# Optimization experiments

Measured on AMD Instinct MI355X. Metric: run time of the kernel, lower is better.

## Reference

```python
import jax, jax.numpy as jnp
import numpy as np

B, N, D, DH = 2, 256, 256, 256


def setup_inputs() -> dict:
    key = jax.random.key(0)
    ks = jax.random.split(key, 8)
    s = 1.0 / np.sqrt(D)
    return {
        "x": jax.random.normal(ks[0], (B, N, D), dtype=jnp.float32),
        "e": jax.random.normal(ks[1], (B, N, N, D), dtype=jnp.float32),
        "Wq": jax.random.normal(ks[2], (D, DH), dtype=jnp.float32) * s,
        "bq": jnp.zeros((DH,), dtype=jnp.float32),
        "Wk": jax.random.normal(ks[3], (D, DH), dtype=jnp.float32) * s,
        "bk": jnp.zeros((DH,), dtype=jnp.float32),
        "Wv": jax.random.normal(ks[4], (D, DH), dtype=jnp.float32) * s,
        "bv": jnp.zeros((DH,), dtype=jnp.float32),
    }


def reference(x, e, Wq, bq, Wk, bk, Wv, bv):
    # Q_edge: [B, N, N, DH]; indexed Q[b, j, i, :]
    Q = jnp.einsum("bjid,dh->bjih", e, Wq) + bq
    K = x @ Wk + bk  # [B, N, DH]
    V = x @ Wv + bv  # [B, N, DH]
    scale = 1.0 / jnp.sqrt(jnp.asarray(Q.shape[-1], Q.dtype))
    # K_i[b,j,i] = K[b,i];  K_j[b,j,i] = K[b,j]  (torch expand semantics)
    att_i = jnp.exp(jnp.einsum("bjih,bih->bji", Q, K) * scale)
    att_j = jnp.exp(jnp.einsum("bjih,bjh->bji", Q, K) * scale)
    att_sum = att_i + att_j
    ai = att_i / att_sum  # dropout with p=0.0 is identity
    aj = att_j / att_sum
    # e_out[b,j,i] = ai*V[b,i] + aj*V[b,j]
    e_out = ai[..., None] * V[:, None, :, :] + aj[..., None] * V[:, :, None, :]
    return (x, e_out)
```

## Files before the change

### kernel.cpp

```cpp
#include <hip/hip_runtime.h>
#include <hip/hip_bf16.h>

constexpr int Bc  = 2;
constexpr int Nc  = 256;
constexpr int Dc  = 256;
constexpr int DHc = 256;
constexpr int BM  = 64;
constexpr int NIB = Nc / BM;

__global__ __launch_bounds__(256)
void prep_gvc(const float* __restrict__ x,
              const float* __restrict__ Wq, const float* __restrict__ bq,
              const float* __restrict__ Wk, const float* __restrict__ bk,
              const float* __restrict__ Wv, const float* __restrict__ bv,
              float* __restrict__ G, float* __restrict__ V, float* __restrict__ cc) {
    constexpr int RPB = 4;
    constexpr float scale = 0.0625f;
    __shared__ float xs[RPB][Dc];
    __shared__ float ks[RPB][DHc];
    const int r0 = blockIdx.x * RPB;
    const int dd = threadIdx.x;

    #pragma unroll
    for (int rr = 0; rr < RPB; ++rr)
        xs[rr][dd] = x[(size_t)(r0 + rr) * Dc + dd];
    __syncthreads();

    float ka[RPB], va[RPB];
    {
        float bkv = bk[dd], bvv = bv[dd];
        #pragma unroll
        for (int rr = 0; rr < RPB; ++rr) { ka[rr] = bkv; va[rr] = bvv; }
    }
    #pragma unroll 4
    for (int d0 = 0; d0 < Dc; ++d0) {
        float wk = Wk[(size_t)d0 * DHc + dd];
        float wv = Wv[(size_t)d0 * DHc + dd];
        #pragma unroll
        for (int rr = 0; rr < RPB; ++rr) {
            ka[rr] += xs[rr][d0] * wk;
            va[rr] += xs[rr][d0] * wv;
        }
    }
    #pragma unroll
    for (int rr = 0; rr < RPB; ++rr) {
        ks[rr][dd] = ka[rr];
        V[(size_t)(r0 + rr) * DHc + dd] = va[rr];
    }
    __syncthreads();

    float ga[RPB] = {};
    #pragma unroll 8
    for (int h = 0; h < DHc; ++h) {
        float wq = Wq[(size_t)dd * DHc + h];
        #pragma unroll
        for (int rr = 0; rr < RPB; ++rr) ga[rr] += ks[rr][h] * wq;
    }
    #pragma unroll
    for (int rr = 0; rr < RPB; ++rr)
        G[(size_t)(r0 + rr) * Dc + dd] = ga[rr] * scale;

    {
        int rr = dd >> 6, l = dd & 63;
        float p = 0.f;
        #pragma unroll
        for (int k = 0; k < 4; ++k) p += ks[rr][l + 64 * k] * bq[l + 64 * k];
        #pragma unroll
        for (int m = 1; m < 64; m <<= 1) p += __shfl_xor(p, m, 64);
        if (l == 0) cc[r0 + rr] = p * scale;
    }
}

__global__ __launch_bounds__(256)
void edge_main(const float* __restrict__ e,
               const float* __restrict__ G,
               const float* __restrict__ V,
               const float* __restrict__ cc,
               float* __restrict__ eout) {
    const int bid = blockIdx.x;
    const int b   = bid / (Nc * NIB);
    const int rem = bid % (Nc * NIB);
    const int j   = rem / NIB;
    const int i0  = (rem % NIB) * BM;
    const int tid = threadIdx.x;
    const int l   = tid & 63;
    const int w   = tid >> 6;

    const size_t nbase = (size_t)b * Nc;
    const float4 gj = *reinterpret_cast<const float4*>(G + (nbase + j) * Dc + l * 4);
    const float4 vj = *reinterpret_cast<const float4*>(V + (nbase + j) * DHc + l * 4);
    const float  cj = cc[nbase + j];

    const int ibase = i0 + w * 16;
    const float4* erow = reinterpret_cast<const float4*>(
        e + (((size_t)b * Nc + j) * Nc + ibase) * Dc) + l;
    const float4* Grow = reinterpret_cast<const float4*>(G + (nbase + ibase) * Dc) + l;
    const float4* Vrow = reinterpret_cast<const float4*>(V + (nbase + ibase) * DHc) + l;
    float4* orow = reinterpret_cast<float4*>(
        eout + (((size_t)b * Nc + j) * Nc + ibase) * Dc) + l;
    const float* ccp = cc + nbase + ibase;

    #pragma unroll 4
    for (int t = 0; t < 16; ++t) {
        float4 ev = erow[(size_t)t * 64];
        float4 gi = Grow[(size_t)t * 64];
        float si = ev.x * gi.x + ev.y * gi.y + ev.z * gi.z + ev.w * gi.w;
        float sj = ev.x * gj.x + ev.y * gj.y + ev.z * gj.z + ev.w * gj.w;
        #pragma unroll
        for (int m = 1; m < 64; m <<= 1) {
            si += __shfl_xor(si, m, 64);
            sj += __shfl_xor(sj, m, 64);
        }
        si += ccp[t];
        sj += cj;
        float ai = 1.f / (1.f + __expf(sj - si));
        float aj = 1.f - ai;
        float4 vi = Vrow[(size_t)t * 64];
        float4 o;
        o.x = ai * vi.x + aj * vj.x;
        o.y = ai * vi.y + aj * vj.y;
        o.z = ai * vi.z + aj * vj.z;
        o.w = ai * vi.w + aj * vj.w;
        orow[(size_t)t * 64] = o;
    }
}

extern "C" void kernel_launch(void* const* d_in, const int* in_sizes, int n_in,
                              void* d_out, int out_size, void* d_ws, size_t ws_size,
                              hipStream_t stream) {
    const float* x  = (const float*)d_in[0];
    const float* e  = (const float*)d_in[1];
    const float* Wq = (const float*)d_in[2];
    const float* bq = (const float*)d_in[3];
    const float* Wk = (const float*)d_in[4];
    const float* bk = (const float*)d_in[5];
    const float* Wv = (const float*)d_in[6];
    const float* bv = (const float*)d_in[7];
    float* out = (float*)d_out;

    float* G  = (float*)d_ws;
    float* V  = G + (size_t)Bc * Nc * Dc;
    float* cc = V + (size_t)Bc * Nc * DHc;

    hipMemcpyAsync(out, x, (size_t)Bc * Nc * Dc * sizeof(float),
                   hipMemcpyDeviceToDevice, stream);

    prep_gvc<<<Bc * Nc / 4, 256, 0, stream>>>(x, Wq, bq, Wk, bk, Wv, bv, G, V, cc);
    edge_main<<<Bc * Nc * NIB, 256, 0, stream>>>(
        e, G, V, cc, out + (size_t)Bc * Nc * Dc);
}
```

Before: 306.6 us.

## Split wavefronts into quarter-row groups with register prefetch and nontemporal stores

Each wavefront now handles four rows at once, with 16 lanes per row holding four float4 chunks each. This shrinks the cross-lane reduction from 6 to 4 shuffle steps. The next rows' e and G values are prefetched into registers while the current row is computed. Outputs are written with nontemporal stores to avoid polluting the cache with streaming data. The device-to-device memcpy of x is replaced by a small copy kernel launched after the main kernel. Together these aim to cut launch/copy overhead and memory latency stalls, at the cost of higher register pressure.

Result: faster. 295.0 us (-3.8%).

```diff
diff --git a/kernel.cpp b/kernel.cpp
--- a/kernel.cpp
+++ b/kernel.cpp
@@ -1,5 +1,7 @@
 #include <hip/hip_runtime.h>
 #include <hip/hip_bf16.h>
+
+typedef float nt4 __attribute__((ext_vector_type(4)));
 
 constexpr int Bc  = 2;
 constexpr int Nc  = 256;
@@ -72,6 +74,12 @@
 }
 
 __global__ __launch_bounds__(256)
+void copy_x(const float4* __restrict__ in, float4* __restrict__ out) {
+    int i = blockIdx.x * 256 + threadIdx.x;
+    out[i] = in[i];
+}
+
+__global__ __launch_bounds__(256)
 void edge_main(const float* __restrict__ e,
                const float* __restrict__ G,
                const float* __restrict__ V,
@@ -85,43 +93,80 @@
     const int tid = threadIdx.x;
     const int l   = tid & 63;
     const int w   = tid >> 6;
+    const int g   = l >> 4;
+    const int c4  = l & 15;
 
     const size_t nbase = (size_t)b * Nc;
-    const float4 gj = *reinterpret_cast<const float4*>(G + (nbase + j) * Dc + l * 4);
-    const float4 vj = *reinterpret_cast<const float4*>(V + (nbase + j) * DHc + l * 4);
-    const float  cj = cc[nbase + j];
+    const float4* G4 = reinterpret_cast<const float4*>(G);
+    const float4* V4 = reinterpret_cast<const float4*>(V);
 
-    const int ibase = i0 + w * 16;
-    const float4* erow = reinterpret_cast<const float4*>(
-        e + (((size_t)b * Nc + j) * Nc + ibase) * Dc) + l;
-    const float4* Grow = reinterpret_cast<const float4*>(G + (nbase + ibase) * Dc) + l;
-    const float4* Vrow = reinterpret_cast<const float4*>(V + (nbase + ibase) * DHc) + l;
-    float4* orow = reinterpret_cast<float4*>(
-        eout + (((size_t)b * Nc + j) * Nc + ibase) * Dc) + l;
-    const float* ccp = cc + nbase + ibase;
+    float4 gj[4], vj[4];
+    #pragma unroll
+    for (int k = 0; k < 4; ++k) {
+        gj[k] = G4[(nbase + j) * 64 + c4 + 16 * k];
+        vj[k] = V4[(nbase + j) * 64 + c4 + 16 * k];
+    }
+    const float cj = cc[nbase + j];
 
-    #pragma unroll 4
-    for (int t = 0; t < 16; ++t) {
-        float4 ev = erow[(size_t)t * 64];
-        float4 gi = Grow[(size_t)t * 64];
-        float si = ev.x * gi.x + ev.y * gi.y + ev.z * gi.z + ev.w * gi.w;
-        float sj = ev.x * gj.x + ev.y * gj.y + ev.z * gj.z + ev.w * gj.w;
+    const int rbase = i0 + w * 16;
+    const float4* e4 = reinterpret_cast<const float4*>(e) +
+                       (((size_t)b * Nc + j) * Nc + rbase) * 64;
+    float4* o4 = reinterpret_cast<float4*>(eout) +
+                 (((size_t)b * Nc + j) * Nc + rbase) * 64;
+    const float4* Gi = G4 + (nbase + rbase) * 64;
+    const float4* Vi = V4 + (nbase + rbase) * 64;
+    const float*  ccp = cc + nbase + rbase;
+
+    float4 ev[4], gi[4];
+    #pragma unroll
+    for (int k = 0; k < 4; ++k) {
+        ev[k] = e4[(size_t)g * 64 + c4 + 16 * k];
+        gi[k] = Gi[(size_t)g * 64 + c4 + 16 * k];
+    }
+
+    #pragma unroll
+    for (int t = 0; t < 4; ++t) {
+        const int r = t * 4 + g;
+        float4 nev[4], ngi[4], vi[4];
+        if (t < 3) {
+            #pragma unroll
+            for (int k = 0; k < 4; ++k) {
+                nev[k] = e4[(size_t)(r + 4) * 64 + c4 + 16 * k];
+                ngi[k] = Gi[(size_t)(r + 4) * 64 + c4 + 16 * k];
+            }
+        }
         #pragma unroll
-        for (int m = 1; m < 64; m <<= 1) {
+        for (int k = 0; k < 4; ++k)
+            vi[k] = Vi[(size_t)r * 64 + c4 + 16 * k];
+
+        float si = 0.f, sj = 0.f;
+        #pragma unroll
+        for (int k = 0; k < 4; ++k) {
+            si += ev[k].x * gi[k].x + ev[k].y * gi[k].y + ev[k].z * gi[k].z + ev[k].w * gi[k].w;
+            sj += ev[k].x * gj[k].x + ev[k].y * gj[k].y + ev[k].z * gj[k].z + ev[k].w * gj[k].w;
+        }
+        #pragma unroll
+        for (int m = 1; m < 16; m <<= 1) {
             si += __shfl_xor(si, m, 64);
             sj += __shfl_xor(sj, m, 64);
         }
-        si += ccp[t];
+        si += ccp[r];
         sj += cj;
         float ai = 1.f / (1.f + __expf(sj - si));
         float aj = 1.f - ai;
-        float4 vi = Vrow[(size_t)t * 64];
-        float4 o;
-        o.x = ai * vi.x + aj * vj.x;
-        o.y = ai * vi.y + aj * vj.y;
-        o.z = ai * vi.z + aj * vj.z;
-        o.w = ai * vi.w + aj * vj.w;
-        orow[(size_t)t * 64] = o;
+
+        #pragma unroll
+        for (int k = 0; k < 4; ++k) {
+            nt4 o;
+            o.x = ai * vi[k].x + aj * vj[k].x;
+            o.y = ai * vi[k].y + aj * vj[k].y;
+            o.z = ai * vi[k].z + aj * vj[k].z;
+            o.w = ai * vi[k].w + aj * vj[k].w;
+            __builtin_nontemporal_store(
+                o, reinterpret_cast<nt4*>(&o4[(size_t)r * 64 + c4 + 16 * k]));
+        }
+        #pragma unroll
+        for (int k = 0; k < 4; ++k) { ev[k] = nev[k]; gi[k] = ngi[k]; }
     }
 }
 
@@ -142,10 +187,9 @@
     float* V  = G + (size_t)Bc * Nc * Dc;
     float* cc = V + (size_t)Bc * Nc * DHc;
 
-    hipMemcpyAsync(out, x, (size_t)Bc * Nc * Dc * sizeof(float),
-                   hipMemcpyDeviceToDevice, stream);
-
     prep_gvc<<<Bc * Nc / 4, 256, 0, stream>>>(x, Wq, bq, Wk, bk, Wv, bv, G, V, cc);
     edge_main<<<Bc * Nc * NIB, 256, 0, stream>>>(
         e, G, V, cc, out + (size_t)Bc * Nc * Dc);
+    copy_x<<<(Bc * Nc * Dc / 4) / 256, 256, 0, stream>>>(
+        (const float4*)x, (float4*)out);
 }
```

## Remap edge kernel to 16 lanes per row with nontemporal stores and kernel copy

Applied to the files above, without the earlier changes.

Each 64-lane wave now handles four i rows at once, with 16 lanes per row. All e, G and V loads are issued up front, so the 6-step shuffle reduction over 64 lanes becomes a 4-step reduction over 16 lanes and many more loads are in flight. Output writes use nontemporal stores to avoid polluting cache with the streamed 134MB result. The hipMemcpyAsync for x is replaced by a small copy kernel launched after the main kernel, removing the memcpy call's overhead. The grid grows to 16 rows per block, so there are 4x as many blocks.

Measured after the change: 288.0 us. -6.1%, faster.

```diff
diff --git a/kernel.cpp b/kernel.cpp
--- a/kernel.cpp
+++ b/kernel.cpp
@@ -1,12 +1,12 @@
 #include <hip/hip_runtime.h>
 #include <hip/hip_bf16.h>
+
+typedef float nt4 __attribute__((ext_vector_type(4)));
 
 constexpr int Bc  = 2;
 constexpr int Nc  = 256;
 constexpr int Dc  = 256;
 constexpr int DHc = 256;
-constexpr int BM  = 64;
-constexpr int NIB = Nc / BM;
 
 __global__ __launch_bounds__(256)
 void prep_gvc(const float* __restrict__ x,
@@ -72,57 +72,85 @@
 }
 
 __global__ __launch_bounds__(256)
+void copy_x(const float4* __restrict__ in, float4* __restrict__ out) {
+    int i = blockIdx.x * 256 + threadIdx.x;
+    out[i] = in[i];
+}
+
+__global__ __launch_bounds__(256)
 void edge_main(const float* __restrict__ e,
                const float* __restrict__ G,
                const float* __restrict__ V,
                const float* __restrict__ cc,
                float* __restrict__ eout) {
     const int bid = blockIdx.x;
-    const int b   = bid / (Nc * NIB);
-    const int rem = bid % (Nc * NIB);
-    const int j   = rem / NIB;
-    const int i0  = (rem % NIB) * BM;
+    const int b   = bid >> 12;
+    const int rem = bid & 4095;
+    const int j   = rem >> 4;
+    const int i0  = (rem & 15) << 4;
     const int tid = threadIdx.x;
     const int l   = tid & 63;
     const int w   = tid >> 6;
+    const int g   = l >> 4;
+    const int c4  = l & 15;
+    const int i   = i0 + w * 4 + g;
 
-    const size_t nbase = (size_t)b * Nc;
-    const float4 gj = *reinterpret_cast<const float4*>(G + (nbase + j) * Dc + l * 4);
-    const float4 vj = *reinterpret_cast<const float4*>(V + (nbase + j) * DHc + l * 4);
-    const float  cj = cc[nbase + j];
+    const size_t nb = (size_t)b * Nc;
+    const float4* G4 = reinterpret_cast<const float4*>(G);
+    const float4* V4 = reinterpret_cast<const float4*>(V);
+    const float4* e4 = reinterpret_cast<const float4*>(e) +
+                       (((size_t)b * Nc + j) * Nc + i) * 64;
+    float4* o4 = reinterpret_cast<float4*>(eout) +
+                 (((size_t)b * Nc + j) * Nc + i) * 64;
 
-    const int ibase = i0 + w * 16;
-    const float4* erow = reinterpret_cast<const float4*>(
-        e + (((size_t)b * Nc + j) * Nc + ibase) * Dc) + l;
-    const float4* Grow = reinterpret_cast<const float4*>(G + (nbase + ibase) * Dc) + l;
-    const float4* Vrow = reinterpret_cast<const float4*>(V + (nbase + ibase) * DHc) + l;
-    float4* orow = reinterpret_cast<float4*>(
-        eout + (((size_t)b * Nc + j) * Nc + ibase) * Dc) + l;
-    const float* ccp = cc + nbase + ibase;
+    float4 ev0 = e4[c4], ev1 = e4[c4 + 16], ev2 = e4[c4 + 32], ev3 = e4[c4 + 48];
 
-    #pragma unroll 4
-    for (int t = 0; t < 16; ++t) {
-        float4 ev = erow[(size_t)t * 64];
-        float4 gi = Grow[(size_t)t * 64];
-        float si = ev.x * gi.x + ev.y * gi.y + ev.z * gi.z + ev.w * gi.w;
-        float sj = ev.x * gj.x + ev.y * gj.y + ev.z * gj.z + ev.w * gj.w;
-        #pragma unroll
-        for (int m = 1; m < 64; m <<= 1) {
-            si += __shfl_xor(si, m, 64);
-            sj += __shfl_xor(sj, m, 64);
-        }
-        si += ccp[t];
-        sj += cj;
-        float ai = 1.f / (1.f + __expf(sj - si));
-        float aj = 1.f - ai;
-        float4 vi = Vrow[(size_t)t * 64];
-        float4 o;
-        o.x = ai * vi.x + aj * vj.x;
-        o.y = ai * vi.y + aj * vj.y;
-        o.z = ai * vi.z + aj * vj.z;
-        o.w = ai * vi.w + aj * vj.w;
-        orow[(size_t)t * 64] = o;
+    const float4* Gi = G4 + (nb + i) * 64;
+    const float4* Gj = G4 + (nb + j) * 64;
+    const float4* Vi = V4 + (nb + i) * 64;
+    const float4* Vj = V4 + (nb + j) * 64;
+    float4 gi0 = Gi[c4], gi1 = Gi[c4 + 16], gi2 = Gi[c4 + 32], gi3 = Gi[c4 + 48];
+    float4 gj0 = Gj[c4], gj1 = Gj[c4 + 16], gj2 = Gj[c4 + 32], gj3 = Gj[c4 + 48];
+    float4 vi0 = Vi[c4], vi1 = Vi[c4 + 16], vi2 = Vi[c4 + 32], vi3 = Vi[c4 + 48];
+    float4 vj0 = Vj[c4], vj1 = Vj[c4 + 16], vj2 = Vj[c4 + 32], vj3 = Vj[c4 + 48];
+    const float ci = cc[nb + i];
+    const float cj = cc[nb + j];
+
+    float si, sj;
+    {
+        float a, bdot;
+        a  = ev0.x * gi0.x + ev0.y * gi0.y + ev0.z * gi0.z + ev0.w * gi0.w;
+        a += ev1.x * gi1.x + ev1.y * gi1.y + ev1.z * gi1.z + ev1.w * gi1.w;
+        a += ev2.x * gi2.x + ev2.y * gi2.y + ev2.z * gi2.z + ev2.w * gi2.w;
+        a += ev3.x * gi3.x + ev3.y * gi3.y + ev3.z * gi3.z + ev3.w * gi3.w;
+        bdot  = ev0.x * gj0.x + ev0.y * gj0.y + ev0.z * gj0.z + ev0.w * gj0.w;
+        bdot += ev1.x * gj1.x + ev1.y * gj1.y + ev1.z * gj1.z + ev1.w * gj1.w;
+        bdot += ev2.x * gj2.x + ev2.y * gj2.y + ev2.z * gj2.z + ev2.w * gj2.w;
+        bdot += ev3.x * gj3.x + ev3.y * gj3.y + ev3.z * gj3.z + ev3.w * gj3.w;
+        si = a; sj = bdot;
     }
+    #pragma unroll
+    for (int m = 1; m < 16; m <<= 1) {
+        si += __shfl_xor(si, m, 64);
+        sj += __shfl_xor(sj, m, 64);
+    }
+    si += ci;
+    sj += cj;
+    const float ai = 1.f / (1.f + __expf(sj - si));
+    const float aj = 1.f - ai;
+
+    nt4 o;
+    #define EMIT(VI, VJ, OFF)                                   \
+        o.x = ai * VI.x + aj * VJ.x;                            \
+        o.y = ai * VI.y + aj * VJ.y;                            \
+        o.z = ai * VI.z + aj * VJ.z;                            \
+        o.w = ai * VI.w + aj * VJ.w;                            \
+        __builtin_nontemporal_store(o, reinterpret_cast<nt4*>(&o4[OFF]));
+    EMIT(vi0, vj0, c4)
+    EMIT(vi1, vj1, c4 + 16)
+    EMIT(vi2, vj2, c4 + 32)
+    EMIT(vi3, vj3, c4 + 48)
+    #undef EMIT
 }
 
 extern "C" void kernel_launch(void* const* d_in, const int* in_sizes, int n_in,
@@ -142,10 +170,9 @@
     float* V  = G + (size_t)Bc * Nc * Dc;
     float* cc = V + (size_t)Bc * Nc * DHc;
 
-    hipMemcpyAsync(out, x, (size_t)Bc * Nc * Dc * sizeof(float),
-                   hipMemcpyDeviceToDevice, stream);
-
     prep_gvc<<<Bc * Nc / 4, 256, 0, stream>>>(x, Wq, bq, Wk, bk, Wv, bv, G, V, cc);
-    edge_main<<<Bc * Nc * NIB, 256, 0, stream>>>(
+    edge_main<<<Bc * Nc * Nc / 16, 256, 0, stream>>>(
         e, G, V, cc, out + (size_t)Bc * Nc * Dc);
+    copy_x<<<(Bc * Nc * Dc / 4) / 256, 256, 0, stream>>>(
+        (const float4*)x, (float4*)out);
 }
```

## Fuse x copy into prep kernel, prefetch edge rows, use nontemporal stores

Applied to the files above, without the earlier changes.

The separate device-to-device memcpy of x is dropped and the copy is done inside prep_gvc as it loads x. edge_main now gives each wavefront 32 consecutive i rows and software-prefetches the next e/G/V/cc values one iteration ahead, so load latency overlaps the shuffle reductions. Output writes use nontemporal stores to avoid polluting cache with the large streaming output. Launch bounds are raised for occupancy; the register cost of the full unroll with prefetch may limit it.

New measurement: 295.8 us. -3.5%, faster.

```diff
diff --git a/kernel.cpp b/kernel.cpp
--- a/kernel.cpp
+++ b/kernel.cpp
@@ -1,19 +1,20 @@
 #include <hip/hip_runtime.h>
 #include <hip/hip_bf16.h>
+
+typedef float nt4 __attribute__((ext_vector_type(4)));
 
 constexpr int Bc  = 2;
 constexpr int Nc  = 256;
 constexpr int Dc  = 256;
 constexpr int DHc = 256;
-constexpr int BM  = 64;
-constexpr int NIB = Nc / BM;
 
 __global__ __launch_bounds__(256)
 void prep_gvc(const float* __restrict__ x,
               const float* __restrict__ Wq, const float* __restrict__ bq,
               const float* __restrict__ Wk, const float* __restrict__ bk,
               const float* __restrict__ Wv, const float* __restrict__ bv,
-              float* __restrict__ G, float* __restrict__ V, float* __restrict__ cc) {
+              float* __restrict__ G, float* __restrict__ V, float* __restrict__ cc,
+              float* __restrict__ xout) {
     constexpr int RPB = 4;
     constexpr float scale = 0.0625f;
     __shared__ float xs[RPB][Dc];
@@ -22,8 +23,11 @@
     const int dd = threadIdx.x;
 
     #pragma unroll
-    for (int rr = 0; rr < RPB; ++rr)
-        xs[rr][dd] = x[(size_t)(r0 + rr) * Dc + dd];
+    for (int rr = 0; rr < RPB; ++rr) {
+        float xv = x[(size_t)(r0 + rr) * Dc + dd];
+        xs[rr][dd] = xv;
+        xout[(size_t)(r0 + rr) * Dc + dd] = xv;
+    }
     __syncthreads();
 
     float ka[RPB], va[RPB];
@@ -71,39 +75,49 @@
     }
 }
 
-__global__ __launch_bounds__(256)
+__global__ __launch_bounds__(256, 4)
 void edge_main(const float* __restrict__ e,
                const float* __restrict__ G,
                const float* __restrict__ V,
                const float* __restrict__ cc,
                float* __restrict__ eout) {
-    const int bid = blockIdx.x;
-    const int b   = bid / (Nc * NIB);
-    const int rem = bid % (Nc * NIB);
-    const int j   = rem / NIB;
-    const int i0  = (rem % NIB) * BM;
-    const int tid = threadIdx.x;
-    const int l   = tid & 63;
-    const int w   = tid >> 6;
+    const int W = blockIdx.x * 4 + (threadIdx.x >> 6);
+    const int l = threadIdx.x & 63;
+    const int b   = W >> 11;
+    const int rem = W & 2047;
+    const int j   = rem >> 3;
+    const int s   = rem & 7;
+    const int i0  = s * 32;
 
-    const size_t nbase = (size_t)b * Nc;
-    const float4 gj = *reinterpret_cast<const float4*>(G + (nbase + j) * Dc + l * 4);
-    const float4 vj = *reinterpret_cast<const float4*>(V + (nbase + j) * DHc + l * 4);
-    const float  cj = cc[nbase + j];
+    const size_t nb = (size_t)b * Nc;
+    const float4* G4 = reinterpret_cast<const float4*>(G);
+    const float4* V4 = reinterpret_cast<const float4*>(V);
 
-    const int ibase = i0 + w * 16;
-    const float4* erow = reinterpret_cast<const float4*>(
-        e + (((size_t)b * Nc + j) * Nc + ibase) * Dc) + l;
-    const float4* Grow = reinterpret_cast<const float4*>(G + (nbase + ibase) * Dc) + l;
-    const float4* Vrow = reinterpret_cast<const float4*>(V + (nbase + ibase) * DHc) + l;
-    float4* orow = reinterpret_cast<float4*>(
-        eout + (((size_t)b * Nc + j) * Nc + ibase) * Dc) + l;
-    const float* ccp = cc + nbase + ibase;
+    const float4 gj = G4[(nb + j) * 64 + l];
+    const float4 vj = V4[(nb + j) * 64 + l];
+    const float  cj = cc[nb + j];
 
-    #pragma unroll 4
-    for (int t = 0; t < 16; ++t) {
-        float4 ev = erow[(size_t)t * 64];
-        float4 gi = Grow[(size_t)t * 64];
+    const float4* e4 = reinterpret_cast<const float4*>(e) +
+                       (((size_t)b * Nc + j) * Nc + i0) * 64 + l;
+    float4* o4 = reinterpret_cast<float4*>(eout) +
+                 (((size_t)b * Nc + j) * Nc + i0) * 64 + l;
+    const float4* Gi = G4 + (nb + i0) * 64 + l;
+    const float4* Vi = V4 + (nb + i0) * 64 + l;
+    const float*  ccp = cc + nb + i0;
+
+    float4 ev = e4[0], gi = Gi[0], vi = Vi[0];
+    float  ci = ccp[0];
+
+    #pragma unroll
+    for (int t = 0; t < 32; ++t) {
+        float4 nev, ngi, nvi;
+        float  nci;
+        if (t < 31) {
+            nev = e4[(size_t)(t + 1) * 64];
+            ngi = Gi[(size_t)(t + 1) * 64];
+            nvi = Vi[(size_t)(t + 1) * 64];
+            nci = ccp[t + 1];
+        }
         float si = ev.x * gi.x + ev.y * gi.y + ev.z * gi.z + ev.w * gi.w;
         float sj = ev.x * gj.x + ev.y * gj.y + ev.z * gj.z + ev.w * gj.w;
         #pragma unroll
@@ -111,17 +125,19 @@
             si += __shfl_xor(si, m, 64);
             sj += __shfl_xor(sj, m, 64);
         }
-        si += ccp[t];
+        si += ci;
         sj += cj;
-        float ai = 1.f / (1.f + __expf(sj - si));
-        float aj = 1.f - ai;
-        float4 vi = Vrow[(size_t)t * 64];
-        float4 o;
+        const float ai = 1.f / (1.f + __expf(sj - si));
+        const float aj = 1.f - ai;
+
+        nt4 o;
         o.x = ai * vi.x + aj * vj.x;
         o.y = ai * vi.y + aj * vj.y;
         o.z = ai * vi.z + aj * vj.z;
         o.w = ai * vi.w + aj * vj.w;
-        orow[(size_t)t * 64] = o;
+        __builtin_nontemporal_store(o, reinterpret_cast<nt4*>(&o4[(size_t)t * 64]));
+
+        ev = nev; gi = ngi; vi = nvi; ci = nci;
     }
 }
 
@@ -142,10 +158,8 @@
     float* V  = G + (size_t)Bc * Nc * Dc;
     float* cc = V + (size_t)Bc * Nc * DHc;
 
-    hipMemcpyAsync(out, x, (size_t)Bc * Nc * Dc * sizeof(float),
-                   hipMemcpyDeviceToDevice, stream);
-
-    prep_gvc<<<Bc * Nc / 4, 256, 0, stream>>>(x, Wq, bq, Wk, bk, Wv, bv, G, V, cc);
-    edge_main<<<Bc * Nc * NIB, 256, 0, stream>>>(
+    prep_gvc<<<Bc * Nc / 4, 256, 0, stream>>>(x, Wq, bq, Wk, bk, Wv, bv,
+                                              G, V, cc, out);
+    edge_main<<<Bc * Nc * 8 / 4, 256, 0, stream>>>(
         e, G, V, cc, out + (size_t)Bc * Nc * Dc);
 }
```
